# Kernel tuning notes

Hardware: AMD Instinct MI355X
Metric: run time of the kernel (lower is better)

Reference implementation:

```python
import jax, jax.numpy as jnp
import numpy as np

N = 131072          # total atoms/nodes
LSQ = 9             # (lmax+1)^2 spherical coefficients
C = 128             # sphere_channels
H = 1024            # hidden_channels
NUM_MOLS = 2048     # number of molecules (len(natoms))


def setup_inputs() -> dict:
    key = jax.random.key(0)
    ks = jax.random.split(key, 8)
    node_embedding = jax.random.normal(ks[0], (N, LSQ, C), dtype=jnp.float32)
    batch = jnp.sort(jax.random.randint(ks[1], (N,), 0, NUM_MOLS, dtype=jnp.int64))
    natoms = jax.random.randint(ks[2], (NUM_MOLS,), 1, 100, dtype=jnp.int64)
    # MLP parameters (Linear weights stored as [in, out] for x @ W + b)
    s1 = 1.0 / np.sqrt(C)
    s2 = 1.0 / np.sqrt(H)
    W1 = jax.random.uniform(ks[3], (C, H), jnp.float32, -s1, s1)
    b1 = jnp.zeros((H,), jnp.float32)
    W2 = jax.random.uniform(ks[4], (H, H), jnp.float32, -s2, s2)
    b2 = jnp.zeros((H,), jnp.float32)
    W3 = jax.random.uniform(ks[5], (H, 1), jnp.float32, -s2, s2)
    b3 = jnp.zeros((1,), jnp.float32)
    return {"node_embedding": node_embedding, "W1": W1, "b1": b1,
            "W2": W2, "b2": b2, "W3": W3, "b3": b3,
            "batch": batch, "natoms": natoms}


def reference(node_embedding, W1, b1, W2, b2, W3, b3, batch, natoms):
    # take l=0 coefficient: [N, C]
    x = node_embedding[:, 0, :]
    h = jax.nn.silu(x @ W1 + b1)          # [N, H]
    h = jax.nn.silu(h @ W2 + b2)          # [N, H]
    node_energy = (h @ W3 + b3)[:, 0]     # [N]
    # scatter-sum per molecule (index_add_)
    energy = jax.ops.segment_sum(node_energy, batch, num_segments=NUM_MOLS)
    return energy  # reduce == 'sum'
```

## Files before the change

### kernel.cpp

```cpp
#include <hip/hip_runtime.h>

typedef unsigned short u16;
typedef __attribute__((ext_vector_type(8)))  short bf16x8;
typedef __attribute__((ext_vector_type(16))) float f32x16;

#define NROWS 131072
#define NMOL  2048
#define CIN   128
#define HDIM  1024
#define BM    64
#define EMBSTRIDE 1152

#define KT1 (CIN  / 16)
#define KT2 (HDIM / 16)
#define NT  (HDIM / 32)

__device__ __forceinline__ u16 f2bf(float f) {
    union { float f; unsigned u; } v; v.f = f;
    unsigned u = v.u;
    u += 0x7FFFu + ((u >> 16) & 1u);
    return (u16)(u >> 16);
}

__device__ __forceinline__ float silu_f(float v) {
    float e = __expf(-v);
    return v * __builtin_amdgcn_rcpf(1.0f + e);
}

__device__ __forceinline__ f32x16 mfma32(bf16x8 a, bf16x8 b, f32x16 c) {
    return __builtin_amdgcn_mfma_f32_32x32x16_bf16(a, b, c, 0, 0, 0);
}

__global__ void pack_w32(const float* __restrict__ W, u16* __restrict__ dst, int K, int N) {
    int tid  = blockIdx.x * blockDim.x + threadIdx.x;
    int lane = tid & 63;
    int frag = tid >> 6;
    int NTl = N >> 5;
    int KTl = K >> 4;
    if (frag >= KTl * NTl) return;
    int kt = frag / NTl;
    int nt = frag - kt * NTl;
    int col  = (nt << 5) + (lane & 31);
    int krow = (kt << 4) + ((lane >> 5) << 3);
    __align__(16) u16 tmp[8];
    #pragma unroll
    for (int j = 0; j < 8; ++j) tmp[j] = f2bf(W[(size_t)(krow + j) * N + col]);
    *reinterpret_cast<uint4*>(dst + (size_t)tid * 8) = *reinterpret_cast<uint4*>(tmp);
}

__global__ __launch_bounds__(512, 2) void fused_mlp(
    const float* __restrict__ emb,
    const u16*  __restrict__ w1f,
    const u16*  __restrict__ w2f,
    const float* __restrict__ b1,
    const float* __restrict__ b2,
    const float* __restrict__ w3,
    const float* __restrict__ b3,
    float* __restrict__ node_e)
{
    __shared__ u16  x_lds[BM][CIN + 8];
    __shared__ u16  h1_lds[BM][HDIM + 8];
    __shared__ float e_red[8][BM];

    const int tid  = threadIdx.x;
    const int lane = tid & 63;
    const int w    = tid >> 6;
    const int l31  = lane & 31;
    const int lhi  = lane >> 5;
    const int row0 = blockIdx.x * BM;

    {
        int r   = tid >> 3;
        int seg = tid & 7;
        const float4* s4 = reinterpret_cast<const float4*>(
            emb + (size_t)(row0 + r) * EMBSTRIDE + seg * 16);
        __align__(16) u16 u[16];
        #pragma unroll
        for (int i = 0; i < 4; ++i) {
            float4 f = s4[i];
            u[i*4+0] = f2bf(f.x); u[i*4+1] = f2bf(f.y);
            u[i*4+2] = f2bf(f.z); u[i*4+3] = f2bf(f.w);
        }
        uint4* d = reinterpret_cast<uint4*>(&x_lds[r][seg * 16]);
        d[0] = reinterpret_cast<uint4*>(u)[0];
        d[1] = reinterpret_cast<uint4*>(u)[1];
    }

    auto LDB1 = [&](int kt, bf16x8* b) {
        #pragma unroll
        for (int nti = 0; nti < 4; ++nti)
            b[nti] = *reinterpret_cast<const bf16x8*>(
                w1f + (((size_t)kt * NT + w * 4 + nti) * 64 + lane) * 8);
    };
    auto LDB2 = [&](int kt, bf16x8* b) {
        #pragma unroll
        for (int nti = 0; nti < 4; ++nti)
            b[nti] = *reinterpret_cast<const bf16x8*>(
                w2f + (((size_t)kt * NT + w * 4 + nti) * 64 + lane) * 8);
    };

    bf16x8 bC[4], bN[4];
    LDB1(0, bC);
    __syncthreads();

    {
        f32x16 acc1[2][4];
        #pragma unroll
        for (int mt = 0; mt < 2; ++mt)
            #pragma unroll
            for (int nti = 0; nti < 4; ++nti)
                #pragma unroll
                for (int r = 0; r < 16; ++r) acc1[mt][nti][r] = 0.0f;

        #pragma unroll
        for (int kt = 0; kt < KT1; ++kt) {
            if (kt + 1 < KT1) LDB1(kt + 1, bN);
            bf16x8 a[2];
            #pragma unroll
            for (int mt = 0; mt < 2; ++mt)
                a[mt] = *reinterpret_cast<const bf16x8*>(
                    &x_lds[mt*32 + l31][kt*16 + (lhi << 3)]);
            #pragma unroll
            for (int nti = 0; nti < 4; ++nti)
                #pragma unroll
                for (int mt = 0; mt < 2; ++mt)
                    acc1[mt][nti] = mfma32(a[mt], bC[nti], acc1[mt][nti]);
            if (kt + 1 < KT1) {
                #pragma unroll
                for (int i = 0; i < 4; ++i) bC[i] = bN[i];
            }
        }

        #pragma unroll
        for (int nti = 0; nti < 4; ++nti) {
            int col = w*128 + nti*32 + l31;
            float bias = b1[col];
            #pragma unroll
            for (int mt = 0; mt < 2; ++mt)
                #pragma unroll
                for (int r = 0; r < 16; ++r) {
                    int row = mt*32 + (r & 3) + 8*(r >> 2) + 4*lhi;
                    h1_lds[row][col] = f2bf(silu_f(acc1[mt][nti][r] + bias));
                }
        }
    }

    LDB2(0, bC);
    LDB2(1, bN);
    __syncthreads();

    auto LDA2 = [&](int kt, bf16x8* a) {
        #pragma unroll
        for (int mt = 0; mt < 2; ++mt)
            a[mt] = *reinterpret_cast<const bf16x8*>(
                &h1_lds[mt*32 + l31][kt*16 + (lhi << 3)]);
    };

    f32x16 acc[2][4];
    #pragma unroll
    for (int mt = 0; mt < 2; ++mt)
        #pragma unroll
        for (int nti = 0; nti < 4; ++nti)
            #pragma unroll
            for (int r = 0; r < 16; ++r) acc[mt][nti][r] = 0.0f;

    bf16x8 aC[2], aN[2];
    LDA2(0, aC);
    LDA2(1, aN);

    #pragma unroll 4
    for (int kt = 0; kt < KT2 - 2; kt += 2) {
        bf16x8 aP[2], bP[4];
        LDB2(kt + 2, bP);
        LDA2(kt + 2, aP);
        #pragma unroll
        for (int nti = 0; nti < 4; ++nti)
            #pragma unroll
            for (int mt = 0; mt < 2; ++mt)
                acc[mt][nti] = mfma32(aC[mt], bC[nti], acc[mt][nti]);
        bf16x8 aQ[2], bQ[4];
        LDB2(kt + 3, bQ);
        LDA2(kt + 3, aQ);
        #pragma unroll
        for (int nti = 0; nti < 4; ++nti)
            #pragma unroll
            for (int mt = 0; mt < 2; ++mt)
                acc[mt][nti] = mfma32(aN[mt], bN[nti], acc[mt][nti]);
        #pragma unroll
        for (int i = 0; i < 2; ++i) { aC[i] = aP[i]; aN[i] = aQ[i]; }
        #pragma unroll
        for (int i = 0; i < 4; ++i) { bC[i] = bP[i]; bN[i] = bQ[i]; }
    }
    #pragma unroll
    for (int nti = 0; nti < 4; ++nti)
        #pragma unroll
        for (int mt = 0; mt < 2; ++mt)
            acc[mt][nti] = mfma32(aC[mt], bC[nti], acc[mt][nti]);
    #pragma unroll
    for (int nti = 0; nti < 4; ++nti)
        #pragma unroll
        for (int mt = 0; mt < 2; ++mt)
            acc[mt][nti] = mfma32(aN[mt], bN[nti], acc[mt][nti]);

    float e_lane[32];
    #pragma unroll
    for (int i = 0; i < 32; ++i) e_lane[i] = 0.0f;

    #pragma unroll
    for (int nti = 0; nti < 4; ++nti) {
        int col = w*128 + nti*32 + l31;
        float bias = b2[col];
        float w3v  = w3[col];
        #pragma unroll
        for (int mt = 0; mt < 2; ++mt)
            #pragma unroll
            for (int r = 0; r < 16; ++r) {
                float s = silu_f(acc[mt][nti][r] + bias);
                e_lane[mt*16 + r] += s * w3v;
            }
    }

    #pragma unroll
    for (int off = 1; off < 32; off <<= 1)
        #pragma unroll
        for (int i = 0; i < 32; ++i)
            e_lane[i] += __shfl_xor(e_lane[i], off, 64);

    if (l31 == 0) {
        #pragma unroll
        for (int mt = 0; mt < 2; ++mt)
            #pragma unroll
            for (int r = 0; r < 16; ++r) {
                int row = mt*32 + (r & 3) + 8*(r >> 2) + 4*lhi;
                e_red[w][row] = e_lane[mt*16 + r];
            }
    }
    __syncthreads();

    if (tid < BM) {
        float s = 0.0f;
        #pragma unroll
        for (int ww = 0; ww < 8; ++ww) s += e_red[ww][tid];
        node_e[row0 + tid] = s + b3[0];
    }
}

__global__ void segsum(const float* __restrict__ node_e,
                       const int* __restrict__ batch,
                       float* __restrict__ out)
{
    int mol  = blockIdx.x;
    int lane = threadIdx.x;

    int lo = 0, hi = NROWS;
    while (lo < hi) { int mid = (lo + hi) >> 1; if (batch[mid] < mol)     lo = mid + 1; else hi = mid; }
    int start = lo;
    lo = start; hi = NROWS;
    while (lo < hi) { int mid = (lo + hi) >> 1; if (batch[mid] < mol + 1) lo = mid + 1; else hi = mid; }
    int end = lo;

    float s = 0.0f;
    for (int i = start + lane; i < end; i += 64) s += node_e[i];
    #pragma unroll
    for (int off = 32; off; off >>= 1) s += __shfl_xor(s, off, 64);
    if (lane == 0) out[mol] = s;
}

extern "C" void kernel_launch(void* const* d_in, const int* in_sizes, int n_in,
                              void* d_out, int out_size, void* d_ws, size_t ws_size,
                              hipStream_t stream) {
    const float* emb = (const float*)d_in[0];
    const float* W1  = (const float*)d_in[1];
    const float* b1  = (const float*)d_in[2];
    const float* W2  = (const float*)d_in[3];
    const float* b2  = (const float*)d_in[4];
    const float* W3  = (const float*)d_in[5];
    const float* b3  = (const float*)d_in[6];
    const int*   batch = (const int*)d_in[7];

    u16* w1f = (u16*)d_ws;
    u16* w2f = (u16*)((char*)d_ws + (size_t)CIN * HDIM * 2);
    float* node_e = (float*)((char*)d_ws + (size_t)CIN * HDIM * 2 + (size_t)HDIM * HDIM * 2);

    pack_w32<<<64,  256, 0, stream>>>(W1, w1f, CIN,  HDIM);
    pack_w32<<<512, 256, 0, stream>>>(W2, w2f, HDIM, HDIM);
    fused_mlp<<<NROWS / BM, 512, 0, stream>>>(emb, w1f, w2f, b1, b2, W3, b3, node_e);
    segsum<<<NMOL, 64, 0, stream>>>(node_e, batch, (float*)d_out);
}
```

Measured before the change: 364.9 us.

## Split fused MLP across 16 waves per block with narrower per-wave column tiles

Doubles the fused MLP block to 1024 threads so each of 16 waves owns 64 output columns instead of 128. This halves per-wave accumulators and B-fragment registers, and puts more waves in flight per CU to hide global and LDS latency. The layer-1 loop now prefetches two k-steps ahead, and the layer-2 loop becomes a single-step rotating pipeline. In exchange, each MFMA now needs twice as many A-fragment LDS reads. The aggressive launch bounds may also squeeze the register budget enough to cause spills.

```diff
diff --git a/kernel.cpp b/kernel.cpp
--- a/kernel.cpp
+++ b/kernel.cpp
@@ -48,7 +48,7 @@
     *reinterpret_cast<uint4*>(dst + (size_t)tid * 8) = *reinterpret_cast<uint4*>(tmp);
 }
 
-__global__ __launch_bounds__(512, 2) void fused_mlp(
+__global__ __launch_bounds__(1024, 4) void fused_mlp(
     const float* __restrict__ emb,
     const u16*  __restrict__ w1f,
     const u16*  __restrict__ w2f,
@@ -60,7 +60,7 @@
 {
     __shared__ u16  x_lds[BM][CIN + 8];
     __shared__ u16  h1_lds[BM][HDIM + 8];
-    __shared__ float e_red[8][BM];
+    __shared__ float e_red[16][BM];
 
     const int tid  = threadIdx.x;
     const int lane = tid & 63;
@@ -70,70 +70,65 @@
     const int row0 = blockIdx.x * BM;
 
     {
-        int r   = tid >> 3;
-        int seg = tid & 7;
+        int r   = tid >> 4;
+        int seg = tid & 15;
         const float4* s4 = reinterpret_cast<const float4*>(
-            emb + (size_t)(row0 + r) * EMBSTRIDE + seg * 16);
-        __align__(16) u16 u[16];
-        #pragma unroll
-        for (int i = 0; i < 4; ++i) {
-            float4 f = s4[i];
-            u[i*4+0] = f2bf(f.x); u[i*4+1] = f2bf(f.y);
-            u[i*4+2] = f2bf(f.z); u[i*4+3] = f2bf(f.w);
-        }
-        uint4* d = reinterpret_cast<uint4*>(&x_lds[r][seg * 16]);
-        d[0] = reinterpret_cast<uint4*>(u)[0];
-        d[1] = reinterpret_cast<uint4*>(u)[1];
+            emb + (size_t)(row0 + r) * EMBSTRIDE + seg * 8);
+        float4 f0 = s4[0], f1 = s4[1];
+        __align__(16) u16 u[8];
+        u[0] = f2bf(f0.x); u[1] = f2bf(f0.y); u[2] = f2bf(f0.z); u[3] = f2bf(f0.w);
+        u[4] = f2bf(f1.x); u[5] = f2bf(f1.y); u[6] = f2bf(f1.z); u[7] = f2bf(f1.w);
+        *reinterpret_cast<uint4*>(&x_lds[r][seg * 8]) = *reinterpret_cast<uint4*>(u);
     }
 
     auto LDB1 = [&](int kt, bf16x8* b) {
         #pragma unroll
-        for (int nti = 0; nti < 4; ++nti)
+        for (int nti = 0; nti < 2; ++nti)
             b[nti] = *reinterpret_cast<const bf16x8*>(
-                w1f + (((size_t)kt * NT + w * 4 + nti) * 64 + lane) * 8);
+                w1f + (((size_t)kt * NT + 2 * w + nti) * 64 + lane) * 8);
     };
     auto LDB2 = [&](int kt, bf16x8* b) {
         #pragma unroll
-        for (int nti = 0; nti < 4; ++nti)
+        for (int nti = 0; nti < 2; ++nti)
             b[nti] = *reinterpret_cast<const bf16x8*>(
-                w2f + (((size_t)kt * NT + w * 4 + nti) * 64 + lane) * 8);
+                w2f + (((size_t)kt * NT + 2 * w + nti) * 64 + lane) * 8);
     };
 
-    bf16x8 bC[4], bN[4];
+    bf16x8 bC[2], bN[2];
     LDB1(0, bC);
+    LDB1(1, bN);
     __syncthreads();
 
     {
-        f32x16 acc1[2][4];
-        #pragma unroll
-        for (int mt = 0; mt < 2; ++mt)
-            #pragma unroll
-            for (int nti = 0; nti < 4; ++nti)
+        f32x16 acc1[2][2];
+        #pragma unroll
+        for (int mt = 0; mt < 2; ++mt)
+            #pragma unroll
+            for (int nti = 0; nti < 2; ++nti)
                 #pragma unroll
                 for (int r = 0; r < 16; ++r) acc1[mt][nti][r] = 0.0f;
 
         #pragma unroll
         for (int kt = 0; kt < KT1; ++kt) {
-            if (kt + 1 < KT1) LDB1(kt + 1, bN);
             bf16x8 a[2];
             #pragma unroll
             for (int mt = 0; mt < 2; ++mt)
                 a[mt] = *reinterpret_cast<const bf16x8*>(
                     &x_lds[mt*32 + l31][kt*16 + (lhi << 3)]);
-            #pragma unroll
-            for (int nti = 0; nti < 4; ++nti)
+            bf16x8 bP[2];
+            if (kt + 2 < KT1) LDB1(kt + 2, bP);
+            #pragma unroll
+            for (int nti = 0; nti < 2; ++nti)
                 #pragma unroll
                 for (int mt = 0; mt < 2; ++mt)
                     acc1[mt][nti] = mfma32(a[mt], bC[nti], acc1[mt][nti]);
-            if (kt + 1 < KT1) {
-                #pragma unroll
-                for (int i = 0; i < 4; ++i) bC[i] = bN[i];
-            }
+            #pragma unroll
+            for (int i = 0; i < 2; ++i) { bC[i] = bN[i]; bN[i] = bP[i]; }
         }
 
         #pragma unroll
-        for (int nti = 0; nti < 4; ++nti) {
-            int col = w*128 + nti*32 + l31;
+        for (int nti = 0; nti < 2; ++nti) {
+            int col = w*64 + nti*32 + l31;
             float bias = b1[col];
             #pragma unroll
             for (int mt = 0; mt < 2; ++mt)
@@ -156,11 +151,11 @@
                 &h1_lds[mt*32 + l31][kt*16 + (lhi << 3)]);
     };
 
-    f32x16 acc[2][4];
+    f32x16 acc[2][2];
     #pragma unroll
     for (int mt = 0; mt < 2; ++mt)
         #pragma unroll
-        for (int nti = 0; nti < 4; ++nti)
+        for (int nti = 0; nti < 2; ++nti)
             #pragma unroll
             for (int r = 0; r < 16; ++r) acc[mt][nti][r] = 0.0f;
 
@@ -168,47 +163,40 @@
     LDA2(0, aC);
     LDA2(1, aN);
 
-    #pragma unroll 4
-    for (int kt = 0; kt < KT2 - 2; kt += 2) {
-        bf16x8 aP[2], bP[4];
+    #pragma unroll 8
+    for (int kt = 0; kt < KT2 - 2; ++kt) {
+        bf16x8 aP[2], bP[2];
         LDB2(kt + 2, bP);
         LDA2(kt + 2, aP);
         #pragma unroll
-        for (int nti = 0; nti < 4; ++nti)
+        for (int nti = 0; nti < 2; ++nti)
             #pragma unroll
             for (int mt = 0; mt < 2; ++mt)
                 acc[mt][nti] = mfma32(aC[mt], bC[nti], acc[mt][nti]);
-        bf16x8 aQ[2], bQ[4];
-        LDB2(kt + 3, bQ);
-        LDA2(kt + 3, aQ);
-        #pragma unroll
-        for (int nti = 0; nti < 4; ++nti)
-            #pragma unroll
-            for (int mt = 0; mt < 2; ++mt)
-                acc[mt][nti] = mfma32(aN[mt], bN[nti], acc[mt][nti]);
-        #pragma unroll
-        for (int i = 0; i < 2; ++i) { aC[i] = aP[i]; aN[i] = aQ[i]; }
-        #pragma unroll
-        for (int i = 0; i < 4; ++i) { bC[i] = bP[i]; bN[i] = bQ[i]; }
-    }
-    #pragma unroll
-    for (int nti = 0; nti < 4; ++nti)
-        #pragma unroll
-        for (int mt = 0; mt < 2; ++mt)
-            acc[mt][nti] = mfma32(aC[mt], bC[nti], acc[mt][nti]);
-    #pragma unroll
-    for (int nti = 0; nti < 4; ++nti)
-        #pragma unroll
-        for (int mt = 0; mt < 2; ++mt)
-            acc[mt][nti] = mfma32(aN[mt], bN[nti], acc[mt][nti]);
+        #pragma unroll
+        for (int i = 0; i < 2; ++i) {
+            aC[i] = aN[i]; aN[i] = aP[i];
+            bC[i] = bN[i]; bN[i] = bP[i];
+        }
+    }
+    #pragma unroll
+    for (int s = 0; s < 2; ++s) {
+        #pragma unroll
+        for (int nti = 0; nti < 2; ++nti)
+            #pragma unroll
+            for (int mt = 0; mt < 2; ++mt)
+                acc[mt][nti] = mfma32(aC[mt], bC[nti], acc[mt][nti]);
+        #pragma unroll
+        for (int i = 0; i < 2; ++i) { aC[i] = aN[i]; bC[i] = bN[i]; }
+    }
 
     float e_lane[32];
     #pragma unroll
     for (int i = 0; i < 32; ++i) e_lane[i] = 0.0f;
 
     #pragma unroll
-    for (int nti = 0; nti < 4; ++nti) {
-        int col = w*128 + nti*32 + l31;
+    for (int nti = 0; nti < 2; ++nti) {
+        int col = w*64 + nti*32 + l31;
         float bias = b2[col];
         float w3v  = w3[col];
         #pragma unroll
@@ -240,7 +228,7 @@
     if (tid < BM) {
         float s = 0.0f;
         #pragma unroll
-        for (int ww = 0; ww < 8; ++ww) s += e_red[ww][tid];
+        for (int ww = 0; ww < 16; ++ww) s += e_red[ww][tid];
         node_e[row0 + tid] = s + b3[0];
     }
 }
@@ -284,6 +272,6 @@
 
     pack_w32<<<64,  256, 0, stream>>>(W1, w1f, CIN,  HDIM);
     pack_w32<<<512, 256, 0, stream>>>(W2, w2f, HDIM, HDIM);
-    fused_mlp<<<NROWS / BM, 512, 0, stream>>>(emb, w1f, w2f, b1, b2, W3, b3, node_e);
+    fused_mlp<<<NROWS / BM, 1024, 0, stream>>>(emb, w1f, w2f, b1, b2, W3, b3, node_e);
     segsum<<<NMOL, 64, 0, stream>>>(node_e, batch, (float*)d_out);
 }
```

Result: no change. 368.1 us (+0.9%).

## Hand-pipeline W2 loads with inline asm double buffer and explicit waitcnt

Applied to the files above, without the earlier changes.

Replaces the compiler-scheduled layer-2 GEMM loop with a manually pipelined loop. Each step consumes two k-tiles, and inline-asm global_load_dwordx4 instructions with immediate offsets fill two 8-register B buffers. Explicit s_waitcnt vmcnt, sched_barrier and s_setprio around the MFMA block keep weight loads two steps ahead and give MFMA issue priority. The aim is to hide global load latency and cut address arithmetic. The cost is fragile inline asm, a fixed waitcnt accounting that depends on no other vector-memory ops being in flight, and more live VGPRs.

```diff
diff --git a/kernel.cpp b/kernel.cpp
--- a/kernel.cpp
+++ b/kernel.cpp
@@ -47,6 +47,51 @@
     for (int j = 0; j < 8; ++j) tmp[j] = f2bf(W[(size_t)(krow + j) * N + col]);
     *reinterpret_cast<uint4*>(dst + (size_t)tid * 8) = *reinterpret_cast<uint4*>(tmp);
 }
+
+#define ISSUE_B(buf, vE, vO)                                              \
+  asm volatile(                                                           \
+    "global_load_dwordx4 %0, %8, %10 offset:0\n\t"                        \
+    "global_load_dwordx4 %1, %8, %10 offset:1024\n\t"                     \
+    "global_load_dwordx4 %2, %8, %10 offset:2048\n\t"                     \
+    "global_load_dwordx4 %3, %8, %10 offset:3072\n\t"                     \
+    "global_load_dwordx4 %4, %9, %10 offset:0\n\t"                        \
+    "global_load_dwordx4 %5, %9, %10 offset:1024\n\t"                     \
+    "global_load_dwordx4 %6, %9, %10 offset:2048\n\t"                     \
+    "global_load_dwordx4 %7, %9, %10 offset:3072"                         \
+    : "=v"(buf[0]), "=v"(buf[1]), "=v"(buf[2]), "=v"(buf[3]),             \
+      "=v"(buf[4]), "=v"(buf[5]), "=v"(buf[6]), "=v"(buf[7])              \
+    : "v"(vE), "v"(vO), "s"(w2f)                                          \
+    : "memory")
+
+#define HALF_KT(buf, ktv, OFS)                                                             \
+  {                                                                                        \
+    const int _kt = (ktv);                                                                 \
+    bf16x8 a0 = *reinterpret_cast<const bf16x8*>(&h1_lds[l31     ][_kt*16 + (lhi<<3)]);    \
+    bf16x8 a1 = *reinterpret_cast<const bf16x8*>(&h1_lds[32 + l31][_kt*16 + (lhi<<3)]);    \
+    acc[0][0] = mfma32(a0, buf[OFS+0], acc[0][0]);                                         \
+    acc[1][0] = mfma32(a1, buf[OFS+0], acc[1][0]);                                         \
+    acc[0][1] = mfma32(a0, buf[OFS+1], acc[0][1]);                                         \
+    acc[1][1] = mfma32(a1, buf[OFS+1], acc[1][1]);                                         \
+    acc[0][2] = mfma32(a0, buf[OFS+2], acc[0][2]);                                         \
+    acc[1][2] = mfma32(a1, buf[OFS+2], acc[1][2]);                                         \
+    acc[0][3] = mfma32(a0, buf[OFS+3], acc[0][3]);                                         \
+    acc[1][3] = mfma32(a1, buf[OFS+3], acc[1][3]);                                         \
+  }
+
+#define STEP(buf, sv, WAITN, DO_ISSUE)                                    \
+  {                                                                       \
+    const int _s = (sv);                                                  \
+    asm volatile("s_waitcnt vmcnt(" #WAITN ")" ::: "memory");             \
+    __builtin_amdgcn_sched_barrier(0);                                    \
+    __builtin_amdgcn_s_setprio(1);                                        \
+    HALF_KT(buf, 2*_s,     0)                                             \
+    HALF_KT(buf, 2*_s + 1, 4)                                             \
+    __builtin_amdgcn_s_setprio(0);                                        \
+    if (DO_ISSUE) {                                                       \
+      unsigned _vE = off0 + (unsigned)(_s + 2) * 65536u;                  \
+      ISSUE_B(buf, _vE, _vE + 32768u);                                    \
+    }                                                                     \
+  }
 
 __global__ __launch_bounds__(512, 2) void fused_mlp(
     const float* __restrict__ emb,
@@ -90,13 +135,7 @@
         #pragma unroll
         for (int nti = 0; nti < 4; ++nti)
             b[nti] = *reinterpret_cast<const bf16x8*>(
-                w1f + (((size_t)kt * NT + w * 4 + nti) * 64 + lane) * 8);
-    };
-    auto LDB2 = [&](int kt, bf16x8* b) {
-        #pragma unroll
-        for (int nti = 0; nti < 4; ++nti)
-            b[nti] = *reinterpret_cast<const bf16x8*>(
-                w2f + (((size_t)kt * NT + w * 4 + nti) * 64 + lane) * 8);
+                w1f + (((size_t)kt * NT + 4 * w + nti) * 64 + lane) * 8);
     };
 
     bf16x8 bC[4], bN[4];
@@ -145,62 +184,27 @@
         }
     }
 
-    LDB2(0, bC);
-    LDB2(1, bN);
+    const unsigned off0 = (unsigned)((w << 12) + (lane << 4));
+
+    f32x16 acc[2][4];
+    #pragma unroll
+    for (int mt = 0; mt < 2; ++mt)
+        #pragma unroll
+        for (int nti = 0; nti < 4; ++nti)
+            #pragma unroll
+            for (int r = 0; r < 16; ++r) acc[mt][nti][r] = 0.0f;
+
+    bf16x8 b0[8], b1v[8];
+    ISSUE_B(b0,  off0,           off0 + 32768u);
+    ISSUE_B(b1v, off0 + 65536u,  off0 + 98304u);
     __syncthreads();
 
-    auto LDA2 = [&](int kt, bf16x8* a) {
-        #pragma unroll
-        for (int mt = 0; mt < 2; ++mt)
-            a[mt] = *reinterpret_cast<const bf16x8*>(
-                &h1_lds[mt*32 + l31][kt*16 + (lhi << 3)]);
-    };
-
-    f32x16 acc[2][4];
-    #pragma unroll
-    for (int mt = 0; mt < 2; ++mt)
-        #pragma unroll
-        for (int nti = 0; nti < 4; ++nti)
-            #pragma unroll
-            for (int r = 0; r < 16; ++r) acc[mt][nti][r] = 0.0f;
-
-    bf16x8 aC[2], aN[2];
-    LDA2(0, aC);
-    LDA2(1, aN);
-
-    #pragma unroll 4
-    for (int kt = 0; kt < KT2 - 2; kt += 2) {
-        bf16x8 aP[2], bP[4];
-        LDB2(kt + 2, bP);
-        LDA2(kt + 2, aP);
-        #pragma unroll
-        for (int nti = 0; nti < 4; ++nti)
-            #pragma unroll
-            for (int mt = 0; mt < 2; ++mt)
-                acc[mt][nti] = mfma32(aC[mt], bC[nti], acc[mt][nti]);
-        bf16x8 aQ[2], bQ[4];
-        LDB2(kt + 3, bQ);
-        LDA2(kt + 3, aQ);
-        #pragma unroll
-        for (int nti = 0; nti < 4; ++nti)
-            #pragma unroll
-            for (int mt = 0; mt < 2; ++mt)
-                acc[mt][nti] = mfma32(aN[mt], bN[nti], acc[mt][nti]);
-        #pragma unroll
-        for (int i = 0; i < 2; ++i) { aC[i] = aP[i]; aN[i] = aQ[i]; }
-        #pragma unroll
-        for (int i = 0; i < 4; ++i) { bC[i] = bP[i]; bN[i] = bQ[i]; }
-    }
-    #pragma unroll
-    for (int nti = 0; nti < 4; ++nti)
-        #pragma unroll
-        for (int mt = 0; mt < 2; ++mt)
-            acc[mt][nti] = mfma32(aC[mt], bC[nti], acc[mt][nti]);
-    #pragma unroll
-    for (int nti = 0; nti < 4; ++nti)
-        #pragma unroll
-        for (int mt = 0; mt < 2; ++mt)
-            acc[mt][nti] = mfma32(aN[mt], bN[nti], acc[mt][nti]);
+    for (int s = 0; s < 30; s += 2) {
+        STEP(b0,  s,     8, 1)
+        STEP(b1v, s + 1, 8, 1)
+    }
+    STEP(b0,  30, 8, 0)
+    STEP(b1v, 31, 0, 0)
 
     float e_lane[32];
     #pragma unroll
```

Measured after the change: 337.0 us. 1.08x faster.

## Split fused MLP into GEMM1 pack and 256x256-tiled GEMM2 with LDS staging

Applied to the files above, without the earlier changes.

The fused per-64-row MLP is split in two. One kernel computes layer 1 and writes h1 to global memory in MFMA fragment layout. A second kernel runs layer 2 on 256x256 tiles, staging A and B into double-buffered LDS through global_load_lds and writing per-column-block partial energies. segsum then sums the 8 partial slabs and adds b3. The aim is more reuse of W2 and h1 per tile than the old 64-row blocks that streamed the whole W2. The cost is a 256MB h1 round trip through HBM, larger per-node partial buffers, and two extra kernel launches.

```diff
diff --git a/kernel.cpp b/kernel.cpp
--- a/kernel.cpp
+++ b/kernel.cpp
@@ -8,12 +8,15 @@
 #define NMOL  2048
 #define CIN   128
 #define HDIM  1024
-#define BM    64
 #define EMBSTRIDE 1152
 
 #define KT1 (CIN  / 16)
-#define KT2 (HDIM / 16)
 #define NT  (HDIM / 32)
+
+#define BM2 256
+#define BN2 256
+#define NRB (NROWS / BM2)
+#define NCB (HDIM  / BN2)
 
 __device__ __forceinline__ u16 f2bf(float f) {
     union { float f; unsigned u; } v; v.f = f;
@@ -29,6 +32,13 @@
 
 __device__ __forceinline__ f32x16 mfma32(bf16x8 a, bf16x8 b, f32x16 c) {
     return __builtin_amdgcn_mfma_f32_32x32x16_bf16(a, b, c, 0, 0, 0);
+}
+
+__device__ __forceinline__ void gload_lds16(const u16* g, u16* l) {
+    __builtin_amdgcn_global_load_lds(
+        (const __attribute__((address_space(1))) unsigned int*)g,
+        (__attribute__((address_space(3))) unsigned int*)l,
+        16, 0, 0);
 }
 
 __global__ void pack_w32(const float* __restrict__ W, u16* __restrict__ dst, int K, int N) {
@@ -48,26 +58,21 @@
     *reinterpret_cast<uint4*>(dst + (size_t)tid * 8) = *reinterpret_cast<uint4*>(tmp);
 }
 
-__global__ __launch_bounds__(512, 2) void fused_mlp(
+__global__ __launch_bounds__(512, 2) void gemm1_pack(
     const float* __restrict__ emb,
     const u16*  __restrict__ w1f,
-    const u16*  __restrict__ w2f,
     const float* __restrict__ b1,
-    const float* __restrict__ b2,
-    const float* __restrict__ w3,
-    const float* __restrict__ b3,
-    float* __restrict__ node_e)
+    u16* __restrict__ h1f)
 {
-    __shared__ u16  x_lds[BM][CIN + 8];
-    __shared__ u16  h1_lds[BM][HDIM + 8];
-    __shared__ float e_red[8][BM];
+    __shared__ u16 x_lds[64][CIN + 8];
+    __shared__ u16 h1_lds[64][HDIM + 8];
 
     const int tid  = threadIdx.x;
     const int lane = tid & 63;
     const int w    = tid >> 6;
     const int l31  = lane & 31;
     const int lhi  = lane >> 5;
-    const int row0 = blockIdx.x * BM;
+    const int row0 = blockIdx.x * 64;
 
     {
         int r   = tid >> 3;
@@ -90,125 +95,147 @@
         #pragma unroll
         for (int nti = 0; nti < 4; ++nti)
             b[nti] = *reinterpret_cast<const bf16x8*>(
-                w1f + (((size_t)kt * NT + w * 4 + nti) * 64 + lane) * 8);
-    };
-    auto LDB2 = [&](int kt, bf16x8* b) {
-        #pragma unroll
-        for (int nti = 0; nti < 4; ++nti)
-            b[nti] = *reinterpret_cast<const bf16x8*>(
-                w2f + (((size_t)kt * NT + w * 4 + nti) * 64 + lane) * 8);
+                w1f + (((size_t)kt * NT + 4 * w + nti) * 64 + lane) * 8);
     };
 
     bf16x8 bC[4], bN[4];
     LDB1(0, bC);
     __syncthreads();
 
-    {
-        f32x16 acc1[2][4];
-        #pragma unroll
-        for (int mt = 0; mt < 2; ++mt)
-            #pragma unroll
-            for (int nti = 0; nti < 4; ++nti)
-                #pragma unroll
-                for (int r = 0; r < 16; ++r) acc1[mt][nti][r] = 0.0f;
-
-        #pragma unroll
-        for (int kt = 0; kt < KT1; ++kt) {
-            if (kt + 1 < KT1) LDB1(kt + 1, bN);
-            bf16x8 a[2];
-            #pragma unroll
-            for (int mt = 0; mt < 2; ++mt)
-                a[mt] = *reinterpret_cast<const bf16x8*>(
-                    &x_lds[mt*32 + l31][kt*16 + (lhi << 3)]);
-            #pragma unroll
-            for (int nti = 0; nti < 4; ++nti)
-                #pragma unroll
-                for (int mt = 0; mt < 2; ++mt)
-                    acc1[mt][nti] = mfma32(a[mt], bC[nti], acc1[mt][nti]);
-            if (kt + 1 < KT1) {
-                #pragma unroll
-                for (int i = 0; i < 4; ++i) bC[i] = bN[i];
-            }
-        }
-
-        #pragma unroll
-        for (int nti = 0; nti < 4; ++nti) {
-            int col = w*128 + nti*32 + l31;
-            float bias = b1[col];
-            #pragma unroll
-            for (int mt = 0; mt < 2; ++mt)
-                #pragma unroll
-                for (int r = 0; r < 16; ++r) {
-                    int row = mt*32 + (r & 3) + 8*(r >> 2) + 4*lhi;
-                    h1_lds[row][col] = f2bf(silu_f(acc1[mt][nti][r] + bias));
-                }
-        }
-    }
-
-    LDB2(0, bC);
-    LDB2(1, bN);
-    __syncthreads();
-
-    auto LDA2 = [&](int kt, bf16x8* a) {
+    f32x16 acc1[2][4];
+    #pragma unroll
+    for (int mt = 0; mt < 2; ++mt)
+        #pragma unroll
+        for (int nti = 0; nti < 4; ++nti)
+            #pragma unroll
+            for (int r = 0; r < 16; ++r) acc1[mt][nti][r] = 0.0f;
+
+    #pragma unroll
+    for (int kt = 0; kt < KT1; ++kt) {
+        if (kt + 1 < KT1) LDB1(kt + 1, bN);
+        bf16x8 a[2];
         #pragma unroll
         for (int mt = 0; mt < 2; ++mt)
             a[mt] = *reinterpret_cast<const bf16x8*>(
-                &h1_lds[mt*32 + l31][kt*16 + (lhi << 3)]);
-    };
-
-    f32x16 acc[2][4];
-    #pragma unroll
-    for (int mt = 0; mt < 2; ++mt)
+                &x_lds[mt*32 + l31][kt*16 + (lhi << 3)]);
         #pragma unroll
         for (int nti = 0; nti < 4; ++nti)
             #pragma unroll
-            for (int r = 0; r < 16; ++r) acc[mt][nti][r] = 0.0f;
-
-    bf16x8 aC[2], aN[2];
-    LDA2(0, aC);
-    LDA2(1, aN);
-
-    #pragma unroll 4
-    for (int kt = 0; kt < KT2 - 2; kt += 2) {
-        bf16x8 aP[2], bP[4];
-        LDB2(kt + 2, bP);
-        LDA2(kt + 2, aP);
-        #pragma unroll
-        for (int nti = 0; nti < 4; ++nti)
-            #pragma unroll
             for (int mt = 0; mt < 2; ++mt)
-                acc[mt][nti] = mfma32(aC[mt], bC[nti], acc[mt][nti]);
-        bf16x8 aQ[2], bQ[4];
-        LDB2(kt + 3, bQ);
-        LDA2(kt + 3, aQ);
-        #pragma unroll
-        for (int nti = 0; nti < 4; ++nti)
-            #pragma unroll
-            for (int mt = 0; mt < 2; ++mt)
-                acc[mt][nti] = mfma32(aN[mt], bN[nti], acc[mt][nti]);
-        #pragma unroll
-        for (int i = 0; i < 2; ++i) { aC[i] = aP[i]; aN[i] = aQ[i]; }
-        #pragma unroll
-        for (int i = 0; i < 4; ++i) { bC[i] = bP[i]; bN[i] = bQ[i]; }
-    }
-    #pragma unroll
-    for (int nti = 0; nti < 4; ++nti)
-        #pragma unroll
-        for (int mt = 0; mt < 2; ++mt)
-            acc[mt][nti] = mfma32(aC[mt], bC[nti], acc[mt][nti]);
-    #pragma unroll
-    for (int nti = 0; nti < 4; ++nti)
-        #pragma unroll
-        for (int mt = 0; mt < 2; ++mt)
-            acc[mt][nti] = mfma32(aN[mt], bN[nti], acc[mt][nti]);
-
-    float e_lane[32];
-    #pragma unroll
-    for (int i = 0; i < 32; ++i) e_lane[i] = 0.0f;
+                acc1[mt][nti] = mfma32(a[mt], bC[nti], acc1[mt][nti]);
+        if (kt + 1 < KT1) {
+            #pragma unroll
+            for (int i = 0; i < 4; ++i) bC[i] = bN[i];
+        }
+    }
 
     #pragma unroll
     for (int nti = 0; nti < 4; ++nti) {
         int col = w*128 + nti*32 + l31;
+        float bias = b1[col];
+        #pragma unroll
+        for (int mt = 0; mt < 2; ++mt)
+            #pragma unroll
+            for (int r = 0; r < 16; ++r) {
+                int row = mt*32 + (r & 3) + 8*(r >> 2) + 4*lhi;
+                h1_lds[row][col] = f2bf(silu_f(acc1[mt][nti][r] + bias));
+            }
+    }
+    const size_t rt0 = (size_t)blockIdx.x * 2;
+    #pragma unroll
+    for (int rtl = 0; rtl < 2; ++rtl)
+        #pragma unroll
+        for (int j = 0; j < 8; ++j) {
+            int kt2 = w * 8 + j;
+            bf16x8 v = *reinterpret_cast<const bf16x8*>(
+                &h1_lds[rtl*32 + l31][kt2*16 + (lhi << 3)]);
+            *reinterpret_cast<bf16x8*>(
+                h1f + ((rt0 + rtl)*64 + kt2)*512 + lane*8) = v;
+        }
+}
+
+__global__ __launch_bounds__(512, 2) void gemm2_energy(
+    const u16*  __restrict__ h1f,
+    const u16*  __restrict__ w2f,
+    const float* __restrict__ b2,
+    const float* __restrict__ w3,
+    float* __restrict__ e_part)
+{
+    __shared__ u16 ab[2][64 * 512];
+
+    const int tid  = threadIdx.x;
+    const int lane = tid & 63;
+    const int w    = tid >> 6;
+    const int l31  = lane & 31;
+    const int lhi  = lane >> 5;
+    const int rg   = w >> 1;
+    const int cg   = w & 1;
+
+    const int wg = blockIdx.x;
+    const int rb = (wg & 7) + 8 * ((wg >> 3) >> 2);
+    const int cb = (wg >> 3) & 3;
+
+    auto issue_chunk = [&](int kc, int b) {
+        if (w < 4) {
+            #pragma unroll
+            for (int i = 0; i < 8; ++i) {
+                const u16* src = h1f
+                    + (((size_t)rb * 8 + i) * 64 + (size_t)(kc * 4 + w)) * 512
+                    + lane * 8;
+                gload_lds16(src, &ab[b][(size_t)(w*8 + i) * 512 + lane * 8]);
+            }
+        } else {
+            #pragma unroll
+            for (int i = 0; i < 8; ++i) {
+                const u16* src = w2f
+                    + ((size_t)((kc * 4 + (w - 4)) * 32 + cb * 8 + i)) * 512
+                    + lane * 8;
+                gload_lds16(src, &ab[b][(size_t)(32 + (w-4)*8 + i) * 512 + lane * 8]);
+            }
+        }
+    };
+
+    f32x16 acc[2][4];
+    #pragma unroll
+    for (int mt = 0; mt < 2; ++mt)
+        #pragma unroll
+        for (int nti = 0; nti < 4; ++nti)
+            #pragma unroll
+            for (int r = 0; r < 16; ++r) acc[mt][nti][r] = 0.0f;
+
+    issue_chunk(0, 0);
+    __syncthreads();
+
+    for (int kc = 0; kc < 16; ++kc) {
+        const int b = kc & 1;
+        if (kc + 1 < 16) issue_chunk(kc + 1, b ^ 1);
+        #pragma unroll
+        for (int ktl = 0; ktl < 4; ++ktl) {
+            bf16x8 A0 = *reinterpret_cast<const bf16x8*>(&ab[b][(size_t)(ktl*8 + rg*2    ) * 512 + lane*8]);
+            bf16x8 A1 = *reinterpret_cast<const bf16x8*>(&ab[b][(size_t)(ktl*8 + rg*2 + 1) * 512 + lane*8]);
+            bf16x8 B0 = *reinterpret_cast<const bf16x8*>(&ab[b][(size_t)(32 + ktl*8 + cg*4 + 0) * 512 + lane*8]);
+            bf16x8 B1 = *reinterpret_cast<const bf16x8*>(&ab[b][(size_t)(32 + ktl*8 + cg*4 + 1) * 512 + lane*8]);
+            bf16x8 B2 = *reinterpret_cast<const bf16x8*>(&ab[b][(size_t)(32 + ktl*8 + cg*4 + 2) * 512 + lane*8]);
+            bf16x8 B3 = *reinterpret_cast<const bf16x8*>(&ab[b][(size_t)(32 + ktl*8 + cg*4 + 3) * 512 + lane*8]);
+            acc[0][0] = mfma32(A0, B0, acc[0][0]);
+            acc[1][0] = mfma32(A1, B0, acc[1][0]);
+            acc[0][1] = mfma32(A0, B1, acc[0][1]);
+            acc[1][1] = mfma32(A1, B1, acc[1][1]);
+            acc[0][2] = mfma32(A0, B2, acc[0][2]);
+            acc[1][2] = mfma32(A1, B2, acc[1][2]);
+            acc[0][3] = mfma32(A0, B3, acc[0][3]);
+            acc[1][3] = mfma32(A1, B3, acc[1][3]);
+        }
+        __syncthreads();
+    }
+
+    float e_lane[32];
+    #pragma unroll
+    for (int i = 0; i < 32; ++i) e_lane[i] = 0.0f;
+
+    #pragma unroll
+    for (int nti = 0; nti < 4; ++nti) {
+        int col = cb*256 + cg*128 + nti*32 + l31;
         float bias = b2[col];
         float w3v  = w3[col];
         #pragma unroll
@@ -227,26 +254,20 @@
             e_lane[i] += __shfl_xor(e_lane[i], off, 64);
 
     if (l31 == 0) {
+        const size_t slab = (size_t)(cb*2 + cg) * NROWS;
         #pragma unroll
         for (int mt = 0; mt < 2; ++mt)
             #pragma unroll
             for (int r = 0; r < 16; ++r) {
-                int row = mt*32 + (r & 3) + 8*(r >> 2) + 4*lhi;
-                e_red[w][row] = e_lane[mt*16 + r];
-            }
-    }
-    __syncthreads();
-
-    if (tid < BM) {
-        float s = 0.0f;
-        #pragma unroll
-        for (int ww = 0; ww < 8; ++ww) s += e_red[ww][tid];
-        node_e[row0 + tid] = s + b3[0];
-    }
-}
-
-__global__ void segsum(const float* __restrict__ node_e,
+                int row = rg*64 + mt*32 + (r & 3) + 8*(r >> 2) + 4*lhi;
+                e_part[slab + (size_t)rb*256 + row] = e_lane[mt*16 + r];
+            }
+    }
+}
+
+__global__ void segsum(const float* __restrict__ e_part,
                        const int* __restrict__ batch,
+                       const float* __restrict__ b3,
                        float* __restrict__ out)
 {
     int mol  = blockIdx.x;
@@ -259,8 +280,14 @@
     while (lo < hi) { int mid = (lo + hi) >> 1; if (batch[mid] < mol + 1) lo = mid + 1; else hi = mid; }
     int end = lo;
 
+    float b3v = b3[0];
     float s = 0.0f;
-    for (int i = start + lane; i < end; i += 64) s += node_e[i];
+    for (int i = start + lane; i < end; i += 64) {
+        float v = b3v;
+        #pragma unroll
+        for (int sl = 0; sl < 8; ++sl) v += e_part[(size_t)sl * NROWS + i];
+        s += v;
+    }
     #pragma unroll
     for (int off = 32; off; off >>= 1) s += __shfl_xor(s, off, 64);
     if (lane == 0) out[mol] = s;
@@ -278,12 +305,15 @@
     const float* b3  = (const float*)d_in[6];
     const int*   batch = (const int*)d_in[7];
 
-    u16* w1f = (u16*)d_ws;
-    u16* w2f = (u16*)((char*)d_ws + (size_t)CIN * HDIM * 2);
-    float* node_e = (float*)((char*)d_ws + (size_t)CIN * HDIM * 2 + (size_t)HDIM * HDIM * 2);
+    char* ws = (char*)d_ws;
+    u16*   w1f    = (u16*)ws;
+    u16*   w2f    = (u16*)(ws + 262144);
+    u16*   h1f    = (u16*)(ws + 2359296);
+    float* e_part = (float*)(ws + 2359296 + 268435456);
 
     pack_w32<<<64,  256, 0, stream>>>(W1, w1f, CIN,  HDIM);
     pack_w32<<<512, 256, 0, stream>>>(W2, w2f, HDIM, HDIM);
-    fused_mlp<<<NROWS / BM, 512, 0, stream>>>(emb, w1f, w2f, b1, b2, W3, b3, node_e);
-    segsum<<<NMOL, 64, 0, stream>>>(node_e, batch, (float*)d_out);
-}
+    gemm1_pack<<<NROWS / 64, 512, 0, stream>>>(emb, w1f, b1, h1f);
+    gemm2_energy<<<NRB * NCB, 512, 0, stream>>>(h1f, w2f, b2, W3, e_part);
+    segsum<<<NMOL, 64, 0, stream>>>(e_part, batch, b3, (float*)d_out);
+}
```

After: 422.6 us. 15.8% more time.
